# Kernel optimization log

Hardware: AMD Instinct MI355X
Metric: run time of the kernel (lower is better)

Reference implementation:

```python
import jax, jax.numpy as jnp
import numpy as np

EPS_MSG = 1e-7
EPS_BN = 1e-5


def _seg_softmax(logits, seg, num_segments):
    # logits: [E, D] per-edge logits; softmax over edges sharing the same dst node
    m = jax.ops.segment_max(logits, seg, num_segments=num_segments)
    m = jnp.where(jnp.isfinite(m), m, 0.0)
    e = jnp.exp(logits - m[seg])
    s = jax.ops.segment_sum(e, seg, num_segments=num_segments)
    return e / (s[seg] + 1e-16)


def _batchnorm(h, gamma, beta):
    mu = jnp.mean(h, axis=0)
    var = jnp.var(h, axis=0)
    return (h - mu) * jax.lax.rsqrt(var + EPS_BN) * gamma + beta


def setup_inputs() -> dict:
    key = jax.random.key(0)
    ks = jax.random.split(key, 12)
    N, E, G, D, L = 100000, 600000, 512, 128, 7
    x = jax.random.randint(ks[0], (N, 9), 0, 64, dtype=jnp.int32)
    edge_index = jax.random.randint(ks[1], (2, E), 0, N, dtype=jnp.int32)
    edge_attr = jax.random.randint(ks[2], (E, 3), 0, 8, dtype=jnp.int32)
    batch = jnp.sort(jax.random.randint(ks[3], (N,), 0, G, dtype=jnp.int32))
    rf_pred = jax.random.uniform(ks[4], (G,), dtype=jnp.float32)
    atom_emb = jax.random.normal(ks[5], (9, 64, D), dtype=jnp.float32) * 0.02
    bond_emb = jax.random.normal(ks[6], (3, 8, D), dtype=jnp.float32) * 0.02
    conv_w = jax.random.normal(ks[7], (L, D, D), dtype=jnp.float32) * 0.02
    conv_b = jnp.zeros((L, D), dtype=jnp.float32)
    ts = jnp.ones((L,), dtype=jnp.float32)  # learnable inverse temperatures (init 1/t style)
    gammas = jnp.ones((L, D), dtype=jnp.float32)
    bn_betas = jnp.zeros((L, D), dtype=jnp.float32)
    final_w = jax.random.normal(ks[8], (D, 1), dtype=jnp.float32) * 0.02
    final_b = jnp.zeros((1,), dtype=jnp.float32)
    beta = jnp.array([0.5], dtype=jnp.float32)
    return {"x": x, "edge_index": edge_index, "edge_attr": edge_attr, "batch": batch,
            "rf_pred": rf_pred, "atom_emb": atom_emb, "bond_emb": bond_emb,
            "conv_w": conv_w, "conv_b": conv_b, "ts": ts, "gammas": gammas,
            "bn_betas": bn_betas, "final_w": final_w, "final_b": final_b, "beta": beta}


def reference(x, edge_index, edge_attr, batch, rf_pred, atom_emb, bond_emb,
              conv_w, conv_b, ts, gammas, bn_betas, final_w, final_b, beta):
    N = x.shape[0]
    G = rf_pred.shape[0]
    L = conv_w.shape[0]
    src, dst = edge_index[0], edge_index[1]

    # AtomEncoder / BondEncoder: sum of per-feature embeddings
    h = jax.vmap(lambda tab, idx: tab[idx], in_axes=(0, 1))(atom_emb, x).sum(0)          # [N, D]
    e_emb = jax.vmap(lambda tab, idx: tab[idx], in_axes=(0, 1))(bond_emb, edge_attr).sum(0)  # [E, D]

    def genconv(l, hin):
        msg = jax.nn.relu(hin[src] + e_emb) + EPS_MSG          # [E, D]
        alpha = _seg_softmax(msg * ts[l], dst, N)              # softmax aggregation weights
        aggr = jax.ops.segment_sum(alpha * msg, dst, num_segments=N)  # [N, D]
        return (hin + aggr) @ conv_w[l] + conv_b[l]

    # res+ DeeperGCN
    h = genconv(0, h)
    for l in range(1, L):
        h2 = jax.nn.relu(_batchnorm(h, gammas[l - 1], bn_betas[l - 1]))
        h = genconv(l, h2) + h
    h = jax.nn.relu(_batchnorm(h, gammas[L - 1], bn_betas[L - 1]))

    # mean graph pooling
    counts = jnp.maximum(jax.ops.segment_sum(jnp.ones((N,), h.dtype), batch, num_segments=G), 1.0)
    hg = jax.ops.segment_sum(h, batch, num_segments=G) / counts[:, None]  # [G, D]

    dgcn_pred = hg @ final_w + final_b  # [G, 1]
    return (1.0 - beta) * jax.nn.sigmoid(dgcn_pred) + beta * rf_pred.reshape(-1, 1)
```

## Files before the change

### kernel.cpp

```cpp
#include <hip/hip_runtime.h>
#include <hip/hip_fp16.h>
#include <math.h>

#define D 128
#define PF 8

typedef _Float16 f16x8 __attribute__((ext_vector_type(8)));
typedef float f32x4_t __attribute__((ext_vector_type(4)));


__global__ void hist_kernel(const int* __restrict__ edge_index, int* __restrict__ deg, int E) {
    int e = blockIdx.x * blockDim.x + threadIdx.x;
    if (e >= E) return;
    atomicAdd(&deg[edge_index[E + e]], 1);
}

__global__ void scanA_kernel(const int* __restrict__ deg, int* __restrict__ bsum, int n) {
    __shared__ int red[256];
    int b = blockIdx.x, t = threadIdx.x;
    int base = b * 1024 + t * 4;
    int s = 0;
#pragma unroll
    for (int j = 0; j < 4; ++j)
        if (base + j < n) s += deg[base + j];
    red[t] = s;
    __syncthreads();
    for (int off = 128; off > 0; off >>= 1) {
        if (t < off) red[t] += red[t + off];
        __syncthreads();
    }
    if (t == 0) bsum[b] = red[0];
}

__global__ void scanB_kernel(int* __restrict__ bsum, int nb) {
    __shared__ int sh[256];
    int t = threadIdx.x;
    sh[t] = (t < nb) ? bsum[t] : 0;
    __syncthreads();
    for (int off = 1; off < 256; off <<= 1) {
        int v = (t >= off) ? sh[t - off] : 0;
        __syncthreads();
        sh[t] += v;
        __syncthreads();
    }
    if (t < nb) bsum[t] = (t == 0) ? 0 : sh[t - 1];
}

__global__ void scanC_kernel(const int* __restrict__ deg, const int* __restrict__ boff,
                             int* __restrict__ row_start, int n) {
    __shared__ int sh[256];
    int b = blockIdx.x, t = threadIdx.x;
    int base = b * 1024 + t * 4;
    int v[4];
#pragma unroll
    for (int j = 0; j < 4; ++j) v[j] = (base + j < n) ? deg[base + j] : 0;
    int p[4];
    p[0] = 0; p[1] = v[0]; p[2] = v[0] + v[1]; p[3] = v[0] + v[1] + v[2];
    int s = p[3] + v[3];
    sh[t] = s;
    __syncthreads();
    for (int off = 1; off < 256; off <<= 1) {
        int x = (t >= off) ? sh[t - off] : 0;
        __syncthreads();
        sh[t] += x;
        __syncthreads();
    }
    int off0 = boff[b] + sh[t] - s;
#pragma unroll
    for (int j = 0; j < 4; ++j)
        if (base + j < n) row_start[base + j] = off0 + p[j];
    if (base <= n - 1 && n - 1 < base + 4) row_start[n] = off0 + s;
}

__global__ void scatter_kernel(const int* __restrict__ edge_index, const int* __restrict__ edge_attr,
                               int* __restrict__ cursor, int2* __restrict__ csr, int E) {
    int e = blockIdx.x * blockDim.x + threadIdx.x;
    if (e >= E) return;
    int src = edge_index[e];
    int dst = edge_index[E + e];
    int pos = atomicAdd(&cursor[dst], 1);
    int a0 = edge_attr[e * 3], a1 = edge_attr[e * 3 + 1], a2 = edge_attr[e * 3 + 2];
    csr[pos] = make_int2(src, a0 | (a1 << 3) | (a2 << 6));
}

__global__ void ev_build_kernel(const float* __restrict__ bond_emb, __half2* __restrict__ evt) {
    int idx = blockIdx.x * blockDim.x + threadIdx.x;
    if (idx >= 512 * 64) return;
    int combo = idx >> 6, j = idx & 63;
    int d0 = 2 * j;
    float ex = bond_emb[(combo & 7) * D + d0] +
               bond_emb[(8 + ((combo >> 3) & 7)) * D + d0] +
               bond_emb[(16 + ((combo >> 6) & 7)) * D + d0];
    float ey = bond_emb[(combo & 7) * D + d0 + 1] +
               bond_emb[(8 + ((combo >> 3) & 7)) * D + d0 + 1] +
               bond_emb[(16 + ((combo >> 6) & 7)) * D + d0 + 1];
    evt[idx] = __floats2half2_rn(ex, ey);
}

__global__ void wt_build_kernel(const float* __restrict__ conv_w, _Float16* __restrict__ wt,
                                int total) {
    int idx = blockIdx.x * blockDim.x + threadIdx.x;
    if (idx >= total) return;
    int l = idx >> 14;
    int rem = idx & 16383;
    int n = rem >> 7, k = rem & 127;
    wt[idx] = (_Float16)conv_w[(l << 14) + k * 128 + n];
}

__global__ void gstart_kernel(const int* __restrict__ batch, int* __restrict__ gstart,
                              int N, int G) {
    int n = blockIdx.x * blockDim.x + threadIdx.x;
    if (n >= N) return;
    if (n == 0) {
        for (int g = 0; g <= batch[0]; ++g) gstart[g] = 0;
    } else {
        int b0 = batch[n - 1], b1 = batch[n];
        for (int g = b0 + 1; g <= b1; ++g) gstart[g] = n;
    }
    if (n == N - 1) {
        for (int g = batch[N - 1] + 1; g <= G; ++g) gstart[g] = N;
    }
}


__global__ void atom_embed_kernel(const int* __restrict__ x,
                                  const float* __restrict__ atom_emb,
                                  _Float16* __restrict__ h16, int N) {
    long long idx = (long long)blockIdx.x * blockDim.x + threadIdx.x;
    if (idx >= (long long)N * D) return;
    int n = (int)(idx >> 7);
    int d = (int)(idx & 127);
    float acc = 0.f;
#pragma unroll
    for (int f = 0; f < 9; ++f) {
        int v = x[n * 9 + f];
        acc += atom_emb[(long long)(f * 64 + v) * D + d];
    }
    h16[idx] = (_Float16)acc;
}

__global__ void bn_reduce_finalize_kernel(const float* __restrict__ partial, int nb,
                                          const float* __restrict__ gamma,
                                          const float* __restrict__ bnbeta, float invN,
                                          float* __restrict__ aArr, float* __restrict__ bArr) {
    __shared__ float r1[256], r2[256];
    int d = blockIdx.x, t = threadIdx.x;
    float a1 = 0.f, a2 = 0.f;
    for (int i = t; i < nb; i += 256) {
        a1 += partial[(long long)i * 256 + d];
        a2 += partial[(long long)i * 256 + 128 + d];
    }
    r1[t] = a1; r2[t] = a2;
    __syncthreads();
    for (int off = 128; off > 0; off >>= 1) {
        if (t < off) { r1[t] += r1[t + off]; r2[t] += r2[t + off]; }
        __syncthreads();
    }
    if (t == 0) {
        float mean = r1[0] * invN;
        float var = r2[0] * invN - mean * mean;
        float a = rsqrtf(var + 1e-5f) * gamma[d];
        aArr[d] = a;
        bArr[d] = bnbeta[d] - mean * a;
    }
}

__global__ __launch_bounds__(128, 8) void fused_layer_kernel(
        const __half2* __restrict__ h16c,
        const float* __restrict__ aArr, const float* __restrict__ bArr, int applyBN,
        const float* __restrict__ ts, int l,
        const int* __restrict__ row_start, const int2* __restrict__ csr,
        const __half2* __restrict__ evt,
        const _Float16* __restrict__ wt, const float* __restrict__ bias,
        int residual, _Float16* __restrict__ h16out,
        float* __restrict__ partial, int N) {
    __shared__ __align__(16) char smem[8192];
    _Float16* yh = (_Float16*)smem;
    __half2* tile = (__half2*)smem;

    int t = threadIdx.x;
    int row0 = blockIdx.x * 16;
    int wave = t >> 6;
    int lane = t & 63;
    float tsl = ts[l];
    int a = row0 + wave * 8;

    float2 bnA = make_float2(1.f, 0.f), bnB = make_float2(0.f, 0.f);
    if (applyBN) {
        bnA = ((const float2*)aArr)[lane];
        bnB = ((const float2*)bArr)[lane];
    }

    int rsv = row_start[min(a + min(lane, 8), N)];
    int s0 = __builtin_amdgcn_readlane(rsv, 0);
    int s1 = __builtin_amdgcn_readlane(rsv, 8);

#pragma unroll
    for (int i = 0; i < 8; ++i) {
        int r = a + i;
        float2 hs = make_float2(0.f, 0.f);
        if (r < N) {
            hs = __half22float2(h16c[(size_t)r * 64 + lane]);
            if (applyBN) {
                hs.x = fmaxf(hs.x * bnA.x + bnB.x, 0.f);
                hs.y = fmaxf(hs.y * bnA.y + bnB.y, 0.f);
            }
        }
        tile[(wave * 8 + i) * 68 + lane] = __floats2half2_rn(hs.x, hs.y);
    }

    int c0 = s0;
    int2 ea = make_int2(0, 0);
    if (c0 + lane < s1) ea = csr[c0 + lane];

    __half2 hvS[PF], evS[PF];
#pragma unroll
    for (int k = 0; k < PF; ++k) {
        int pp = s0 + k;
        if (pp < s1) {
            int q = pp - c0;
            int srcp = __builtin_amdgcn_readlane(ea.x, q);
            int cbp = __builtin_amdgcn_readlane(ea.y, q);
            hvS[k] = h16c[(size_t)srcp * 64 + lane];
            evS[k] = evt[(size_t)cbp * 64 + lane];
        }
    }

    int cur = 0;
    int nend = __builtin_amdgcn_readlane(rsv, min(cur + 1, 8));
    while (cur < 8 && nend == s0) {
        cur++;
        nend = __builtin_amdgcn_readlane(rsv, min(cur + 1, 8));
    }

    float accwx = 0.f, accwy = 0.f, accmx = 0.f, accmy = 0.f;
    int total = s1 - s0;
    for (int it = 0; it < total; it += PF) {
#pragma unroll
        for (int k = 0; k < PF; ++k) {
            int p = s0 + it + k;
            if (p < s1) {
                float2 hv = __half22float2(hvS[k]);
                float2 ev = __half22float2(evS[k]);
                if (applyBN) {
                    hv.x = fmaxf(hv.x * bnA.x + bnB.x, 0.f);
                    hv.y = fmaxf(hv.y * bnA.y + bnB.y, 0.f);
                }
                float mx = fmaxf(hv.x + ev.x, 0.f) + 1e-7f;
                float my = fmaxf(hv.y + ev.y, 0.f) + 1e-7f;
                float wx = __expf(mx * tsl);
                float wy = __expf(my * tsl);
                accwx += wx; accmx += wx * mx;
                accwy += wy; accmy += wy * my;
                int pp = p + PF;
                if (pp < s1) {
                    if (pp >= c0 + 64) {
                        c0 += 64;
                        ea = (c0 + lane < s1) ? csr[c0 + lane] : make_int2(0, 0);
                    }
                    int q = pp - c0;
                    int srcp = __builtin_amdgcn_readlane(ea.x, q);
                    int cbp = __builtin_amdgcn_readlane(ea.y, q);
                    hvS[k] = h16c[(size_t)srcp * 64 + lane];
                    evS[k] = evt[(size_t)cbp * 64 + lane];
                }
                while (cur < 8 && nend == p + 1) {
                    int slot = (wave * 8 + cur) * 68 + lane;
                    float2 y = __half22float2(tile[slot]);
                    y.x += accmx / (accwx + 1e-16f);
                    y.y += accmy / (accwy + 1e-16f);
                    tile[slot] = __floats2half2_rn(y.x, y.y);
                    accwx = accwy = accmx = accmy = 0.f;
                    cur++;
                    nend = __builtin_amdgcn_readlane(rsv, min(cur + 1, 8));
                }
            }
        }
    }
    __syncthreads();

    int ln = t & 15;
    int quad = (t & 63) >> 4;
    const _Float16* h16in = (const _Float16*)h16c;

    float cs[4] = {0.f, 0.f, 0.f, 0.f};
    float cq[4] = {0.f, 0.f, 0.f, 0.f};
    const _Float16* ap = yh + ln * 136 + quad * 8;
#pragma unroll
    for (int ct = 0; ct < 4; ++ct) {
        int colg = (wave * 4 + ct) * 16 + ln;
        const _Float16* bp = wt + (size_t)colg * 128 + quad * 8;
        f32x4_t c = {0.f, 0.f, 0.f, 0.f};
#pragma unroll
        for (int kk = 0; kk < 4; ++kk) {
            f16x8 av = *(const f16x8*)(ap + kk * 32);
            f16x8 bv = *(const f16x8*)(bp + kk * 32);
            c = __builtin_amdgcn_mfma_f32_16x16x32_f16(av, bv, c, 0, 0, 0);
        }
        float bsv = bias[colg];
#pragma unroll
        for (int reg = 0; reg < 4; ++reg) {
            int r = row0 + quad * 4 + reg;
            if (r < N) {
                long long off = (long long)r * D + colg;
                float o = c[reg] + bsv;
                if (residual) o += (float)h16in[off];
                h16out[off] = (_Float16)o;
                cs[ct] += o; cq[ct] += o * o;
            }
        }
    }

    __syncthreads();
    float* stats = (float*)smem;
    int grp = wave * 4 + quad;
#pragma unroll
    for (int ct = 0; ct < 4; ++ct) {
        int colg = (wave * 4 + ct) * 16 + ln;
        stats[grp * 256 + colg] = cs[ct];
        stats[grp * 256 + 128 + colg] = cq[ct];
    }
    __syncthreads();
    float ssumA = 0.f, ssumB = 0.f;
#pragma unroll
    for (int g = 0; g < 8; ++g) {
        ssumA += stats[g * 256 + t];
        ssumB += stats[g * 256 + 128 + t];
    }
    partial[(long long)blockIdx.x * 256 + t] = ssumA;
    partial[(long long)blockIdx.x * 256 + 128 + t] = ssumB;
}

__global__ void pool_head_kernel(const _Float16* __restrict__ h16, const float* __restrict__ aArr,
                                 const float* __restrict__ bArr, const int* __restrict__ gstart,
                                 const float* __restrict__ fw, const float* __restrict__ fb,
                                 const float* __restrict__ beta, const float* __restrict__ rf,
                                 float* __restrict__ out) {
    __shared__ float red[256];
    int g = blockIdx.x, t = threadIdx.x;
    int d = t & 127, half = t >> 7;
    int s0 = gstart[g], s1 = gstart[g + 1];
    float a = aArr[d], b = bArr[d];
    float acc = 0.f;
    for (int n = s0 + half; n < s1; n += 2)
        acc += fmaxf((float)h16[(long long)n * D + d] * a + b, 0.f);
    red[t] = acc;
    __syncthreads();
    if (t < 128) red[t] += red[t + 128];
    __syncthreads();
    if (t < 64) {
        float v = red[t] * fw[t] + red[t + 64] * fw[t + 64];
#pragma unroll
        for (int off = 32; off > 0; off >>= 1) v += __shfl_down(v, off);
        if (t == 0) {
            float c = fmaxf((float)(s1 - s0), 1.f);
            float pred = v / c + fb[0];
            float sig = 1.f / (1.f + __expf(-pred));
            float bb = beta[0];
            out[g] = (1.f - bb) * sig + bb * rf[g];
        }
    }
}

static inline size_t align16(size_t x) { return (x + 15) & ~(size_t)15; }

extern "C" void kernel_launch(void* const* d_in, const int* in_sizes, int n_in,
                              void* d_out, int out_size, void* d_ws, size_t ws_size,
                              hipStream_t stream) {
    const int* x = (const int*)d_in[0];
    const int* edge_index = (const int*)d_in[1];
    const int* edge_attr = (const int*)d_in[2];
    const int* batch = (const int*)d_in[3];
    const float* rf_pred = (const float*)d_in[4];
    const float* atom_emb = (const float*)d_in[5];
    const float* bond_emb = (const float*)d_in[6];
    const float* conv_w = (const float*)d_in[7];
    const float* conv_b = (const float*)d_in[8];
    const float* ts = (const float*)d_in[9];
    const float* gammas = (const float*)d_in[10];
    const float* bn_betas = (const float*)d_in[11];
    const float* final_w = (const float*)d_in[12];
    const float* final_b = (const float*)d_in[13];
    const float* beta = (const float*)d_in[14];
    float* out = (float*)d_out;

    int N = in_sizes[0] / 9;
    int E = in_sizes[1] / 2;
    int G = in_sizes[4];
    int L = in_sizes[9];

    int mmBlocks = (N + 15) / 16;
    size_t ND = (size_t)N * D;

    char* p = (char*)d_ws;
    _Float16* h16_a = (_Float16*)p;  p += align16(ND * 2);
    _Float16* h16_b = (_Float16*)p;  p += align16(ND * 2);
    __half2* evt = (__half2*)p;      p += align16((size_t)512 * 64 * 4);
    _Float16* wt = (_Float16*)p;     p += align16((size_t)L * 16384 * 2);
    float* partial = (float*)p;      p += align16((size_t)256 * mmBlocks * 4);
    float* aArr = (float*)p;         p += align16((size_t)D * 4);
    float* bArr = (float*)p;         p += align16((size_t)D * 4);
    int* gstart = (int*)p;           p += align16((size_t)(G + 1) * 4);
    int* deg = (int*)p;              p += align16((size_t)N * 4);
    int* row_start = (int*)p;        p += align16((size_t)(N + 1) * 4);
    int* cursor = (int*)p;           p += align16((size_t)N * 4);
    int* bsum = (int*)p;             p += align16((size_t)256 * 4);
    int2* csr = (int2*)p;            p += align16((size_t)E * 8);

    long long ndThreads = (long long)N * D;
    int ndBlocks = (int)((ndThreads + 255) / 256);
    int eBlocks = (E + 255) / 256;
    int nBlocks = (N + 255) / 256;
    int nb1024 = (N + 1023) / 1024;
    int wtTotal = L * 16384;
    float invN = 1.0f / (float)N;

    hipMemsetAsync(deg, 0, (size_t)N * sizeof(int), stream);
    hist_kernel<<<eBlocks, 256, 0, stream>>>(edge_index, deg, E);
    scanA_kernel<<<nb1024, 256, 0, stream>>>(deg, bsum, N);
    scanB_kernel<<<1, 256, 0, stream>>>(bsum, nb1024);
    scanC_kernel<<<nb1024, 256, 0, stream>>>(deg, bsum, row_start, N);
    hipMemcpyAsync(cursor, row_start, (size_t)N * sizeof(int), hipMemcpyDeviceToDevice, stream);
    scatter_kernel<<<eBlocks, 256, 0, stream>>>(edge_index, edge_attr, cursor, csr, E);
    ev_build_kernel<<<(512 * 64 + 255) / 256, 256, 0, stream>>>(bond_emb, evt);
    wt_build_kernel<<<(wtTotal + 255) / 256, 256, 0, stream>>>(conv_w, wt, wtTotal);
    gstart_kernel<<<nBlocks, 256, 0, stream>>>(batch, gstart, N, G);

    atom_embed_kernel<<<ndBlocks, 256, 0, stream>>>(x, atom_emb, h16_a, N);

    _Float16* h16c = h16_a;
    _Float16* h16n = h16_b;
    for (int l = 0; l < L; ++l) {
        int applyBN = (l >= 1) ? 1 : 0;
        if (applyBN) {
            bn_reduce_finalize_kernel<<<128, 256, 0, stream>>>(
                partial, mmBlocks, gammas + (size_t)(l - 1) * D,
                bn_betas + (size_t)(l - 1) * D, invN, aArr, bArr);
        }
        fused_layer_kernel<<<mmBlocks, 128, 0, stream>>>(
            (const __half2*)h16c, aArr, bArr, applyBN, ts, l, row_start, csr, evt,
            wt + (size_t)l * 16384, conv_b + (size_t)l * D,
            applyBN, h16n, partial, N);
        _Float16* tmp16 = h16c; h16c = h16n; h16n = tmp16;
    }

    bn_reduce_finalize_kernel<<<128, 256, 0, stream>>>(
        partial, mmBlocks, gammas + (size_t)(L - 1) * D,
        bn_betas + (size_t)(L - 1) * D, invN, aArr, bArr);
    pool_head_kernel<<<G, 256, 0, stream>>>(h16c, aArr, bArr, gstart,
                                            final_w, final_b, beta, rf_pred, out);
}
```

Baseline: 917.8 us.

## Make fused layer kernel persistent with atomic tile queue and deeper prefetch

The fused GNN layer kernel now runs a capped grid of persistent blocks that pull 16-row tiles from a global atomic counter (one counter per layer, zeroed once), instead of launching one block per tile. The gather prefetch depth is raised from 8 to 12 edges. The aim is to cut block launch and scheduling overhead and balance the irregular per-tile edge counts dynamically. In exchange it adds an atomic, an extra barrier per tile and more registers for the larger prefetch buffers, which may lower occupancy.

```diff
diff --git a/kernel.cpp b/kernel.cpp
--- a/kernel.cpp
+++ b/kernel.cpp
@@ -3,7 +3,7 @@
 #include <math.h>
 
 #define D 128
-#define PF 8
+#define PF 12
 
 typedef _Float16 f16x8 __attribute__((ext_vector_type(8)));
 typedef float f32x4_t __attribute__((ext_vector_type(4)));
@@ -173,17 +173,19 @@
         const __half2* __restrict__ evt,
         const _Float16* __restrict__ wt, const float* __restrict__ bias,
         int residual, _Float16* __restrict__ h16out,
-        float* __restrict__ partial, int N) {
+        float* __restrict__ partial, int* __restrict__ work_ctr, int nTiles, int N) {
     __shared__ __align__(16) char smem[8192];
+    __shared__ int s_tile;
     _Float16* yh = (_Float16*)smem;
     __half2* tile = (__half2*)smem;
 
     int t = threadIdx.x;
-    int row0 = blockIdx.x * 16;
     int wave = t >> 6;
     int lane = t & 63;
+    int ln = t & 15;
+    int quad = (t & 63) >> 4;
     float tsl = ts[l];
-    int a = row0 + wave * 8;
+    const _Float16* h16in = (const _Float16*)h16c;
 
     float2 bnA = make_float2(1.f, 0.f), bnB = make_float2(0.f, 0.f);
     if (applyBN) {
@@ -191,144 +193,150 @@
         bnB = ((const float2*)bArr)[lane];
     }
 
-    int rsv = row_start[min(a + min(lane, 8), N)];
-    int s0 = __builtin_amdgcn_readlane(rsv, 0);
-    int s1 = __builtin_amdgcn_readlane(rsv, 8);
-
-#pragma unroll
-    for (int i = 0; i < 8; ++i) {
-        int r = a + i;
-        float2 hs = make_float2(0.f, 0.f);
-        if (r < N) {
-            hs = __half22float2(h16c[(size_t)r * 64 + lane]);
-            if (applyBN) {
-                hs.x = fmaxf(hs.x * bnA.x + bnB.x, 0.f);
-                hs.y = fmaxf(hs.y * bnA.y + bnB.y, 0.f);
-            }
-        }
-        tile[(wave * 8 + i) * 68 + lane] = __floats2half2_rn(hs.x, hs.y);
-    }
-
-    int c0 = s0;
-    int2 ea = make_int2(0, 0);
-    if (c0 + lane < s1) ea = csr[c0 + lane];
-
-    __half2 hvS[PF], evS[PF];
-#pragma unroll
-    for (int k = 0; k < PF; ++k) {
-        int pp = s0 + k;
-        if (pp < s1) {
-            int q = pp - c0;
-            int srcp = __builtin_amdgcn_readlane(ea.x, q);
-            int cbp = __builtin_amdgcn_readlane(ea.y, q);
-            hvS[k] = h16c[(size_t)srcp * 64 + lane];
-            evS[k] = evt[(size_t)cbp * 64 + lane];
-        }
-    }
-
-    int cur = 0;
-    int nend = __builtin_amdgcn_readlane(rsv, min(cur + 1, 8));
-    while (cur < 8 && nend == s0) {
-        cur++;
-        nend = __builtin_amdgcn_readlane(rsv, min(cur + 1, 8));
-    }
-
-    float accwx = 0.f, accwy = 0.f, accmx = 0.f, accmy = 0.f;
-    int total = s1 - s0;
-    for (int it = 0; it < total; it += PF) {
-#pragma unroll
-        for (int k = 0; k < PF; ++k) {
-            int p = s0 + it + k;
-            if (p < s1) {
-                float2 hv = __half22float2(hvS[k]);
-                float2 ev = __half22float2(evS[k]);
+    for (;;) {
+        if (t == 0) s_tile = atomicAdd(work_ctr, 1);
+        __syncthreads();
+        int tid = s_tile;
+        if (tid >= nTiles) break;
+        int row0 = tid * 16;
+        int a = row0 + wave * 8;
+
+        int rsv = row_start[min(a + min(lane, 8), N)];
+        int s0 = __builtin_amdgcn_readlane(rsv, 0);
+        int s1 = __builtin_amdgcn_readlane(rsv, 8);
+
+#pragma unroll
+        for (int i = 0; i < 8; ++i) {
+            int r = a + i;
+            float2 hs = make_float2(0.f, 0.f);
+            if (r < N) {
+                hs = __half22float2(h16c[(size_t)r * 64 + lane]);
                 if (applyBN) {
-                    hv.x = fmaxf(hv.x * bnA.x + bnB.x, 0.f);
-                    hv.y = fmaxf(hv.y * bnA.y + bnB.y, 0.f);
-                }
-                float mx = fmaxf(hv.x + ev.x, 0.f) + 1e-7f;
-                float my = fmaxf(hv.y + ev.y, 0.f) + 1e-7f;
-                float wx = __expf(mx * tsl);
-                float wy = __expf(my * tsl);
-                accwx += wx; accmx += wx * mx;
-                accwy += wy; accmy += wy * my;
-                int pp = p + PF;
-                if (pp < s1) {
-                    if (pp >= c0 + 64) {
-                        c0 += 64;
-                        ea = (c0 + lane < s1) ? csr[c0 + lane] : make_int2(0, 0);
-                    }
-                    int q = pp - c0;
-                    int srcp = __builtin_amdgcn_readlane(ea.x, q);
-                    int cbp = __builtin_amdgcn_readlane(ea.y, q);
-                    hvS[k] = h16c[(size_t)srcp * 64 + lane];
-                    evS[k] = evt[(size_t)cbp * 64 + lane];
-                }
-                while (cur < 8 && nend == p + 1) {
-                    int slot = (wave * 8 + cur) * 68 + lane;
-                    float2 y = __half22float2(tile[slot]);
-                    y.x += accmx / (accwx + 1e-16f);
-                    y.y += accmy / (accwy + 1e-16f);
-                    tile[slot] = __floats2half2_rn(y.x, y.y);
-                    accwx = accwy = accmx = accmy = 0.f;
-                    cur++;
-                    nend = __builtin_amdgcn_readlane(rsv, min(cur + 1, 8));
+                    hs.x = fmaxf(hs.x * bnA.x + bnB.x, 0.f);
+                    hs.y = fmaxf(hs.y * bnA.y + bnB.y, 0.f);
                 }
             }
-        }
-    }
-    __syncthreads();
-
-    int ln = t & 15;
-    int quad = (t & 63) >> 4;
-    const _Float16* h16in = (const _Float16*)h16c;
-
-    float cs[4] = {0.f, 0.f, 0.f, 0.f};
-    float cq[4] = {0.f, 0.f, 0.f, 0.f};
-    const _Float16* ap = yh + ln * 136 + quad * 8;
-#pragma unroll
-    for (int ct = 0; ct < 4; ++ct) {
-        int colg = (wave * 4 + ct) * 16 + ln;
-        const _Float16* bp = wt + (size_t)colg * 128 + quad * 8;
-        f32x4_t c = {0.f, 0.f, 0.f, 0.f};
-#pragma unroll
-        for (int kk = 0; kk < 4; ++kk) {
-            f16x8 av = *(const f16x8*)(ap + kk * 32);
-            f16x8 bv = *(const f16x8*)(bp + kk * 32);
-            c = __builtin_amdgcn_mfma_f32_16x16x32_f16(av, bv, c, 0, 0, 0);
-        }
-        float bsv = bias[colg];
-#pragma unroll
-        for (int reg = 0; reg < 4; ++reg) {
-            int r = row0 + quad * 4 + reg;
-            if (r < N) {
-                long long off = (long long)r * D + colg;
-                float o = c[reg] + bsv;
-                if (residual) o += (float)h16in[off];
-                h16out[off] = (_Float16)o;
-                cs[ct] += o; cq[ct] += o * o;
+            tile[(wave * 8 + i) * 68 + lane] = __floats2half2_rn(hs.x, hs.y);
+        }
+
+        int c0 = s0;
+        int2 ea = make_int2(0, 0);
+        if (c0 + lane < s1) ea = csr[c0 + lane];
+
+        __half2 hvS[PF], evS[PF];
+#pragma unroll
+        for (int k = 0; k < PF; ++k) {
+            int pp = s0 + k;
+            if (pp < s1) {
+                int q = pp - c0;
+                int srcp = __builtin_amdgcn_readlane(ea.x, q);
+                int cbp = __builtin_amdgcn_readlane(ea.y, q);
+                hvS[k] = h16c[(size_t)srcp * 64 + lane];
+                evS[k] = evt[(size_t)cbp * 64 + lane];
             }
         }
-    }
-
-    __syncthreads();
-    float* stats = (float*)smem;
-    int grp = wave * 4 + quad;
-#pragma unroll
-    for (int ct = 0; ct < 4; ++ct) {
-        int colg = (wave * 4 + ct) * 16 + ln;
-        stats[grp * 256 + colg] = cs[ct];
-        stats[grp * 256 + 128 + colg] = cq[ct];
-    }
-    __syncthreads();
-    float ssumA = 0.f, ssumB = 0.f;
-#pragma unroll
-    for (int g = 0; g < 8; ++g) {
-        ssumA += stats[g * 256 + t];
-        ssumB += stats[g * 256 + 128 + t];
-    }
-    partial[(long long)blockIdx.x * 256 + t] = ssumA;
-    partial[(long long)blockIdx.x * 256 + 128 + t] = ssumB;
+
+        int cur = 0;
+        int nend = __builtin_amdgcn_readlane(rsv, min(cur + 1, 8));
+        while (cur < 8 && nend == s0) {
+            cur++;
+            nend = __builtin_amdgcn_readlane(rsv, min(cur + 1, 8));
+        }
+
+        float accwx = 0.f, accwy = 0.f, accmx = 0.f, accmy = 0.f;
+        int total = s1 - s0;
+        for (int it = 0; it < total; it += PF) {
+#pragma unroll
+            for (int k = 0; k < PF; ++k) {
+                int p = s0 + it + k;
+                if (p < s1) {
+                    float2 hv = __half22float2(hvS[k]);
+                    float2 ev = __half22float2(evS[k]);
+                    if (applyBN) {
+                        hv.x = fmaxf(hv.x * bnA.x + bnB.x, 0.f);
+                        hv.y = fmaxf(hv.y * bnA.y + bnB.y, 0.f);
+                    }
+                    float mx = fmaxf(hv.x + ev.x, 0.f) + 1e-7f;
+                    float my = fmaxf(hv.y + ev.y, 0.f) + 1e-7f;
+                    float wx = __expf(mx * tsl);
+                    float wy = __expf(my * tsl);
+                    accwx += wx; accmx += wx * mx;
+                    accwy += wy; accmy += wy * my;
+                    int pp = p + PF;
+                    if (pp < s1) {
+                        if (pp >= c0 + 64) {
+                            c0 += 64;
+                            ea = (c0 + lane < s1) ? csr[c0 + lane] : make_int2(0, 0);
+                        }
+                        int q = pp - c0;
+                        int srcp = __builtin_amdgcn_readlane(ea.x, q);
+                        int cbp = __builtin_amdgcn_readlane(ea.y, q);
+                        hvS[k] = h16c[(size_t)srcp * 64 + lane];
+                        evS[k] = evt[(size_t)cbp * 64 + lane];
+                    }
+                    while (cur < 8 && nend == p + 1) {
+                        int slot = (wave * 8 + cur) * 68 + lane;
+                        float2 y = __half22float2(tile[slot]);
+                        y.x += accmx / (accwx + 1e-16f);
+                        y.y += accmy / (accwy + 1e-16f);
+                        tile[slot] = __floats2half2_rn(y.x, y.y);
+                        accwx = accwy = accmx = accmy = 0.f;
+                        cur++;
+                        nend = __builtin_amdgcn_readlane(rsv, min(cur + 1, 8));
+                    }
+                }
+            }
+        }
+        __syncthreads();
+
+        float cs[4] = {0.f, 0.f, 0.f, 0.f};
+        float cq[4] = {0.f, 0.f, 0.f, 0.f};
+        const _Float16* ap = yh + ln * 136 + quad * 8;
+#pragma unroll
+        for (int ct = 0; ct < 4; ++ct) {
+            int colg = (wave * 4 + ct) * 16 + ln;
+            const _Float16* bp = wt + (size_t)colg * 128 + quad * 8;
+            f32x4_t c = {0.f, 0.f, 0.f, 0.f};
+#pragma unroll
+            for (int kk = 0; kk < 4; ++kk) {
+                f16x8 av = *(const f16x8*)(ap + kk * 32);
+                f16x8 bv = *(const f16x8*)(bp + kk * 32);
+                c = __builtin_amdgcn_mfma_f32_16x16x32_f16(av, bv, c, 0, 0, 0);
+            }
+            float bsv = bias[colg];
+#pragma unroll
+            for (int reg = 0; reg < 4; ++reg) {
+                int r = row0 + quad * 4 + reg;
+                if (r < N) {
+                    long long off = (long long)r * D + colg;
+                    float o = c[reg] + bsv;
+                    if (residual) o += (float)h16in[off];
+                    h16out[off] = (_Float16)o;
+                    cs[ct] += o; cq[ct] += o * o;
+                }
+            }
+        }
+
+        __syncthreads();
+        float* stats = (float*)smem;
+        int grp = wave * 4 + quad;
+#pragma unroll
+        for (int ct = 0; ct < 4; ++ct) {
+            int colg = (wave * 4 + ct) * 16 + ln;
+            stats[grp * 256 + colg] = cs[ct];
+            stats[grp * 256 + 128 + colg] = cq[ct];
+        }
+        __syncthreads();
+        float ssumA = 0.f, ssumB = 0.f;
+#pragma unroll
+        for (int g = 0; g < 8; ++g) {
+            ssumA += stats[g * 256 + t];
+            ssumB += stats[g * 256 + 128 + t];
+        }
+        partial[(long long)tid * 256 + t] = ssumA;
+        partial[(long long)tid * 256 + 128 + t] = ssumB;
+        __syncthreads();
+    }
 }
 
 __global__ void pool_head_kernel(const _Float16* __restrict__ h16, const float* __restrict__ aArr,
@@ -389,7 +397,7 @@
     int G = in_sizes[4];
     int L = in_sizes[9];
 
-    int mmBlocks = (N + 15) / 16;
+    int nTiles = (N + 15) / 16;
     size_t ND = (size_t)N * D;
 
     char* p = (char*)d_ws;
@@ -397,7 +405,7 @@
     _Float16* h16_b = (_Float16*)p;  p += align16(ND * 2);
     __half2* evt = (__half2*)p;      p += align16((size_t)512 * 64 * 4);
     _Float16* wt = (_Float16*)p;     p += align16((size_t)L * 16384 * 2);
-    float* partial = (float*)p;      p += align16((size_t)256 * mmBlocks * 4);
+    float* partial = (float*)p;      p += align16((size_t)256 * nTiles * 4);
     float* aArr = (float*)p;         p += align16((size_t)D * 4);
     float* bArr = (float*)p;         p += align16((size_t)D * 4);
     int* gstart = (int*)p;           p += align16((size_t)(G + 1) * 4);
@@ -405,6 +413,7 @@
     int* row_start = (int*)p;        p += align16((size_t)(N + 1) * 4);
     int* cursor = (int*)p;           p += align16((size_t)N * 4);
     int* bsum = (int*)p;             p += align16((size_t)256 * 4);
+    int* work_ctr = (int*)p;         p += align16((size_t)L * 4);
     int2* csr = (int2*)p;            p += align16((size_t)E * 8);
 
     long long ndThreads = (long long)N * D;
@@ -416,6 +425,7 @@
     float invN = 1.0f / (float)N;
 
     hipMemsetAsync(deg, 0, (size_t)N * sizeof(int), stream);
+    hipMemsetAsync(work_ctr, 0, (size_t)L * sizeof(int), stream);
     hist_kernel<<<eBlocks, 256, 0, stream>>>(edge_index, deg, E);
     scanA_kernel<<<nb1024, 256, 0, stream>>>(deg, bsum, N);
     scanB_kernel<<<1, 256, 0, stream>>>(bsum, nb1024);
@@ -428,24 +438,25 @@
 
     atom_embed_kernel<<<ndBlocks, 256, 0, stream>>>(x, atom_emb, h16_a, N);
 
+    int fusedGrid = nTiles < 4096 ? nTiles : 4096;
     _Float16* h16c = h16_a;
     _Float16* h16n = h16_b;
     for (int l = 0; l < L; ++l) {
         int applyBN = (l >= 1) ? 1 : 0;
         if (applyBN) {
             bn_reduce_finalize_kernel<<<128, 256, 0, stream>>>(
-                partial, mmBlocks, gammas + (size_t)(l - 1) * D,
+                partial, nTiles, gammas + (size_t)(l - 1) * D,
                 bn_betas + (size_t)(l - 1) * D, invN, aArr, bArr);
         }
-        fused_layer_kernel<<<mmBlocks, 128, 0, stream>>>(
+        fused_layer_kernel<<<fusedGrid, 128, 0, stream>>>(
             (const __half2*)h16c, aArr, bArr, applyBN, ts, l, row_start, csr, evt,
             wt + (size_t)l * 16384, conv_b + (size_t)l * D,
-            applyBN, h16n, partial, N);
+            applyBN, h16n, partial, work_ctr + l, nTiles, N);
         _Float16* tmp16 = h16c; h16c = h16n; h16n = tmp16;
     }
 
     bn_reduce_finalize_kernel<<<128, 256, 0, stream>>>(
-        partial, mmBlocks, gammas + (size_t)(L - 1) * D,
+        partial, nTiles, gammas + (size_t)(L - 1) * D,
         bn_betas + (size_t)(L - 1) * D, invN, aArr, bArr);
     pool_head_kernel<<<G, 256, 0, stream>>>(h16c, aArr, bArr, gstart,
                                             final_w, final_b, beta, rf_pred, out);
```

After: 1.812 ms. +97.4%, slower.

## Schedule layer tiles in descending in-degree order and deepen gather prefetch

Applied to the files above, without the earlier changes.

Adds a counting sort of the 16-row tiles by total in-degree, using a per-tile key histogram, a scan and a scatter. The fused layer kernel then reads its tile index from this order, so heavy tiles launch first, aiming to cut tail imbalance across workgroups. The prefetch depth constant is also raised from 8 to 12. The costs are three small setup kernels, tile order no longer following memory order, and possibly more register pressure from the deeper prefetch.

```diff
diff --git a/kernel.cpp b/kernel.cpp
--- a/kernel.cpp
+++ b/kernel.cpp
@@ -3,7 +3,7 @@
 #include <math.h>
 
 #define D 128
-#define PF 8
+#define PF 12
 
 typedef _Float16 f16x8 __attribute__((ext_vector_type(8)));
 typedef float f32x4_t __attribute__((ext_vector_type(4)));
@@ -122,6 +122,26 @@
     }
 }
 
+__global__ void tile_deg_kernel(const int* __restrict__ row_start, int* __restrict__ tkey,
+                                int* __restrict__ bcnt, int nTiles, int N) {
+    int i = blockIdx.x * blockDim.x + threadIdx.x;
+    if (i >= nTiles) return;
+    int lo = row_start[min(i * 16, N)];
+    int hi = row_start[min(i * 16 + 16, N)];
+    int d = hi - lo;
+    int key = 255 - min(d, 255);
+    tkey[i] = key;
+    atomicAdd(&bcnt[key], 1);
+}
+
+__global__ void tile_scatter_kernel(const int* __restrict__ tkey, int* __restrict__ bcur,
+                                    int* __restrict__ order, int nTiles) {
+    int i = blockIdx.x * blockDim.x + threadIdx.x;
+    if (i >= nTiles) return;
+    int pos = atomicAdd(&bcur[tkey[i]], 1);
+    order[pos] = i;
+}
+
 
 __global__ void atom_embed_kernel(const int* __restrict__ x,
                                   const float* __restrict__ atom_emb,
@@ -170,7 +190,7 @@
         const float* __restrict__ aArr, const float* __restrict__ bArr, int applyBN,
         const float* __restrict__ ts, int l,
         const int* __restrict__ row_start, const int2* __restrict__ csr,
-        const __half2* __restrict__ evt,
+        const __half2* __restrict__ evt, const int* __restrict__ order,
         const _Float16* __restrict__ wt, const float* __restrict__ bias,
         int residual, _Float16* __restrict__ h16out,
         float* __restrict__ partial, int N) {
@@ -179,7 +199,7 @@
     __half2* tile = (__half2*)smem;
 
     int t = threadIdx.x;
-    int row0 = blockIdx.x * 16;
+    int row0 = order[blockIdx.x] * 16;
     int wave = t >> 6;
     int lane = t & 63;
     float tsl = ts[l];
@@ -389,7 +409,7 @@
     int G = in_sizes[4];
     int L = in_sizes[9];
 
-    int mmBlocks = (N + 15) / 16;
+    int nTiles = (N + 15) / 16;
     size_t ND = (size_t)N * D;
 
     char* p = (char*)d_ws;
@@ -397,7 +417,7 @@
     _Float16* h16_b = (_Float16*)p;  p += align16(ND * 2);
     __half2* evt = (__half2*)p;      p += align16((size_t)512 * 64 * 4);
     _Float16* wt = (_Float16*)p;     p += align16((size_t)L * 16384 * 2);
-    float* partial = (float*)p;      p += align16((size_t)256 * mmBlocks * 4);
+    float* partial = (float*)p;      p += align16((size_t)256 * nTiles * 4);
     float* aArr = (float*)p;         p += align16((size_t)D * 4);
     float* bArr = (float*)p;         p += align16((size_t)D * 4);
     int* gstart = (int*)p;           p += align16((size_t)(G + 1) * 4);
@@ -405,6 +425,9 @@
     int* row_start = (int*)p;        p += align16((size_t)(N + 1) * 4);
     int* cursor = (int*)p;           p += align16((size_t)N * 4);
     int* bsum = (int*)p;             p += align16((size_t)256 * 4);
+    int* tkey = (int*)p;             p += align16((size_t)nTiles * 4);
+    int* border = (int*)p;           p += align16((size_t)256 * 4);
+    int* torder = (int*)p;           p += align16((size_t)nTiles * 4);
     int2* csr = (int2*)p;            p += align16((size_t)E * 8);
 
     long long ndThreads = (long long)N * D;
@@ -412,16 +435,21 @@
     int eBlocks = (E + 255) / 256;
     int nBlocks = (N + 255) / 256;
     int nb1024 = (N + 1023) / 1024;
+    int tBlocks = (nTiles + 255) / 256;
     int wtTotal = L * 16384;
     float invN = 1.0f / (float)N;
 
     hipMemsetAsync(deg, 0, (size_t)N * sizeof(int), stream);
+    hipMemsetAsync(border, 0, 256 * sizeof(int), stream);
     hist_kernel<<<eBlocks, 256, 0, stream>>>(edge_index, deg, E);
     scanA_kernel<<<nb1024, 256, 0, stream>>>(deg, bsum, N);
     scanB_kernel<<<1, 256, 0, stream>>>(bsum, nb1024);
     scanC_kernel<<<nb1024, 256, 0, stream>>>(deg, bsum, row_start, N);
     hipMemcpyAsync(cursor, row_start, (size_t)N * sizeof(int), hipMemcpyDeviceToDevice, stream);
     scatter_kernel<<<eBlocks, 256, 0, stream>>>(edge_index, edge_attr, cursor, csr, E);
+    tile_deg_kernel<<<tBlocks, 256, 0, stream>>>(row_start, tkey, border, nTiles, N);
+    scanB_kernel<<<1, 256, 0, stream>>>(border, 256);
+    tile_scatter_kernel<<<tBlocks, 256, 0, stream>>>(tkey, border, torder, nTiles);
     ev_build_kernel<<<(512 * 64 + 255) / 256, 256, 0, stream>>>(bond_emb, evt);
     wt_build_kernel<<<(wtTotal + 255) / 256, 256, 0, stream>>>(conv_w, wt, wtTotal);
     gstart_kernel<<<nBlocks, 256, 0, stream>>>(batch, gstart, N, G);
@@ -434,18 +462,18 @@
         int applyBN = (l >= 1) ? 1 : 0;
         if (applyBN) {
             bn_reduce_finalize_kernel<<<128, 256, 0, stream>>>(
-                partial, mmBlocks, gammas + (size_t)(l - 1) * D,
+                partial, nTiles, gammas + (size_t)(l - 1) * D,
                 bn_betas + (size_t)(l - 1) * D, invN, aArr, bArr);
         }
-        fused_layer_kernel<<<mmBlocks, 128, 0, stream>>>(
-            (const __half2*)h16c, aArr, bArr, applyBN, ts, l, row_start, csr, evt,
+        fused_layer_kernel<<<nTiles, 128, 0, stream>>>(
+            (const __half2*)h16c, aArr, bArr, applyBN, ts, l, row_start, csr, evt, torder,
             wt + (size_t)l * 16384, conv_b + (size_t)l * D,
             applyBN, h16n, partial, N);
         _Float16* tmp16 = h16c; h16c = h16n; h16n = tmp16;
     }
 
     bn_reduce_finalize_kernel<<<128, 256, 0, stream>>>(
-        partial, mmBlocks, gammas + (size_t)(L - 1) * D,
+        partial, nTiles, gammas + (size_t)(L - 1) * D,
         bn_betas + (size_t)(L - 1) * D, invN, aArr, bArr);
     pool_head_kernel<<<G, 256, 0, stream>>>(h16c, aArr, bArr, gstart,
                                             final_w, final_b, beta, rf_pred, out);
```

Result: slower. 938.0 us (+2.2%).
